# Optimization experiments

Measured on AMD Instinct MI355X. Metric: run time of the kernel, lower is better.

Reference implementation:

```python
import math
import jax, jax.numpy as jnp
import numpy as np

NUM_HEADS = 8


def setup_inputs() -> dict:
    key0 = jax.random.key(0)
    ks = jax.random.split(key0, 11)
    R, C, B, E, Q = 64, 1024, 2, 256, 256
    s = 0.05  # keep pre-softmax scores well-conditioned
    return {
        "query": jax.random.normal(ks[0], (B, Q), jnp.float32),
        "key": jax.random.normal(ks[1], (R, C, B, E), jnp.float32),
        "value": jax.random.normal(ks[2], (R, C, B, E), jnp.float32),
        "Wq": jax.random.normal(ks[3], (E, Q), jnp.float32) * s,
        "bq": jax.random.normal(ks[4], (E,), jnp.float32) * s,
        "Wk": jax.random.normal(ks[5], (E, E), jnp.float32) * s,
        "bk": jax.random.normal(ks[6], (E,), jnp.float32) * s,
        "Wv": jax.random.normal(ks[7], (E, E), jnp.float32) * s,
        "bv": jax.random.normal(ks[8], (E,), jnp.float32) * s,
        "Wo": jax.random.normal(ks[9], (E, E), jnp.float32) * s,
        "bo": jax.random.normal(ks[10], (E,), jnp.float32) * s,
    }


def reference(query, key, value, Wq, bq, Wk, bk, Wv, bv, Wo, bo):
    R, C, B, E = key.shape
    H = NUM_HEADS
    D = E // H
    # main (non-chunked) torch path: align_scaling(query) uses query.size(0) == batch_size
    scaling = (D ** -0.5) / math.sqrt(query.shape[0])
    # projections (torch Linear: x @ W.T + b)
    q = (query @ Wq.T + bq).reshape(B, H, D) * scaling          # [B,H,D]
    k = (key @ Wk.T + bk).reshape(R, C, B, H, D)                # [R,C,B,H,D]
    # tied-row scores: contract over rows r AND head_dim d -> [H,B,C]
    attn_weights = jnp.einsum("nhd,rjnhd->hnj", q, k)
    attn_probs = jax.nn.softmax(attn_weights, axis=-1)          # [H,B,C]
    v = (value @ Wv.T + bv).reshape(R, C, B, H, D)              # [R,C,B,H,D]
    # broadcast probs back per row/column (elementwise scale of v)
    context = jnp.einsum("hnj,rjnhd->rjnhd", attn_probs, v)
    context = context.reshape(R, C, B, E)
    output = context @ Wo.T + bo                                 # [R,C,B,E]
    return output, attn_probs
```

## Files before the change

kernel.cpp:

```cpp
#include <hip/hip_runtime.h>

#define R_DIM 64
#define C_DIM 1024
#define B_DIM 2
#define E_DIM 256
#define Q_DIM 256
#define H_DIM 8
#define D_DIM 32
#define ROW_STRIDE ((size_t)C_DIM * B_DIM * E_DIM)
#define LDS_STRIDE 264
#define OS 260
#define OUT_MAIN ((size_t)R_DIM * C_DIM * B_DIM * E_DIM)

typedef short bf16x8 __attribute__((ext_vector_type(8)));
typedef float f32x4 __attribute__((ext_vector_type(4)));

__device__ __forceinline__ unsigned short f2bf(float x) {
  unsigned int u = __builtin_bit_cast(unsigned int, x);
  u += 0x7FFFu + ((u >> 16) & 1u);
  return (unsigned short)(u >> 16);
}

__global__ void prep_q(const float* __restrict__ query, const float* __restrict__ Wq,
                       const float* __restrict__ bq, float* __restrict__ q_out) {
  int idx = blockIdx.x * 256 + threadIdx.x;
  int n = idx >> 8, e = idx & 255;
  const float4* qr = (const float4*)(query + (size_t)n * Q_DIM);
  const float4* wr = (const float4*)(Wq + (size_t)e * Q_DIM);
  float s = bq[e];
#pragma unroll 8
  for (int k = 0; k < Q_DIM / 4; k++) {
    float4 a = qr[k], b = wr[k];
    s += a.x * b.x + a.y * b.y + a.z * b.z + a.w * b.w;
  }
  q_out[idx] = s * 0.125f;
}

__global__ void prep_w(const float* __restrict__ q, const float* __restrict__ Wk,
                       const float* __restrict__ bk, float* __restrict__ w_out,
                       float* __restrict__ bterm_out) {
  int idx = blockIdx.x * 256 + threadIdx.x;
  int e2 = idx & 255;
  int hn = idx >> 8;
  int n = hn & 1, h = hn >> 1;
  float s = 0.f;
#pragma unroll
  for (int d = 0; d < D_DIM; d++)
    s += q[n * E_DIM + h * D_DIM + d] * Wk[(h * D_DIM + d) * E_DIM + e2];
  w_out[idx] = s;
  if (idx < H_DIM * B_DIM) {
    int nn = idx & 1, hh = idx >> 1;
    float sb = 0.f;
#pragma unroll
    for (int d = 0; d < D_DIM; d++)
      sb += q[nn * E_DIM + hh * D_DIM + d] * bk[hh * D_DIM + d];
    bterm_out[idx] = sb;
  }
}

__global__ void prepack(const float* __restrict__ Wv, const float* __restrict__ Wo,
                        unsigned short* __restrict__ B1p, unsigned short* __restrict__ B2p) {
  int gidx = blockIdx.x * blockDim.x + threadIdx.x;
  const float* src = (gidx < 8192) ? Wv : Wo;
  unsigned short* dst = (gidx < 8192) ? B1p : B2p;
  int li = gidx & 8191;
  int lane = li & 63;
  int pk = li >> 6;
  int ntile = pk >> 3, kstep = pk & 7;
  int row = ntile * 16 + (lane & 15);
  int col0 = kstep * 32 + (lane >> 4) * 8;
  for (int jj = 0; jj < 8; jj++)
    dst[li * 8 + jj] = f2bf(src[row * E_DIM + col0 + jj]);
}

__global__ void scores_kernel(const float* __restrict__ key, const float* __restrict__ w,
                              const float* __restrict__ bterm, float* __restrict__ scores) {
  const int bid = blockIdx.x;
  const int j = bid >> 1, n = bid & 1;
  const int e = threadIdx.x;
  const float* kp = key + ((size_t)j * B_DIM + n) * E_DIM + e;
  float ks = 0.f;
#pragma unroll 8
  for (int r = 0; r < R_DIM; r++) ks += kp[(size_t)r * ROW_STRIDE];

  __shared__ float red[H_DIM][4];
  const int lane = e & 63, wv = e >> 6;
  for (int h = 0; h < H_DIM; h++) {
    float p = ks * w[(h * B_DIM + n) * E_DIM + e];
    for (int off = 32; off > 0; off >>= 1) p += __shfl_down(p, off, 64);
    if (lane == 0) red[h][wv] = p;
  }
  __syncthreads();
  if (e < H_DIM) {
    float s = red[e][0] + red[e][1] + red[e][2] + red[e][3] +
              (float)R_DIM * bterm[e * B_DIM + n];
    scores[(e * B_DIM + n) * C_DIM + j] = s;
  }
}

__global__ void softmax_kernel(const float* __restrict__ scores, float* __restrict__ probs,
                               float* __restrict__ probs_out) {
  const int hn = blockIdx.x;
  const int t = threadIdx.x;
  const float* s = scores + (size_t)hn * C_DIM;
  float v[4];
  float mx = -1e30f;
  for (int i = 0; i < 4; i++) {
    v[i] = s[t + i * 256];
    mx = fmaxf(mx, v[i]);
  }
  __shared__ float sm[4];
  const int lane = t & 63, wv = t >> 6;
  for (int off = 32; off > 0; off >>= 1) mx = fmaxf(mx, __shfl_down(mx, off, 64));
  if (lane == 0) sm[wv] = mx;
  __syncthreads();
  mx = fmaxf(fmaxf(sm[0], sm[1]), fmaxf(sm[2], sm[3]));
  float sum = 0.f;
  for (int i = 0; i < 4; i++) {
    v[i] = expf(v[i] - mx);
    sum += v[i];
  }
  for (int off = 32; off > 0; off >>= 1) sum += __shfl_down(sum, off, 64);
  __syncthreads();
  if (lane == 0) sm[wv] = sum;
  __syncthreads();
  sum = sm[0] + sm[1] + sm[2] + sm[3];
  float inv = 1.0f / sum;
  for (int i = 0; i < 4; i++) {
    float p = v[i] * inv;
    probs[(size_t)hn * C_DIM + t + i * 256] = p;
    probs_out[(size_t)hn * C_DIM + t + i * 256] = p;
  }
}

union SmemT {
  unsigned short tile[64 * LDS_STRIDE];
  float otile[32 * OS];
};

__global__ __launch_bounds__(256, 4) void fused_pv(
    const float* __restrict__ value, const unsigned short* __restrict__ B1p,
    const unsigned short* __restrict__ B2p, const float* __restrict__ bv,
    const float* __restrict__ bo, const float* __restrict__ probs,
    float* __restrict__ out) {
  __shared__ SmemT sm;
  const int bid = blockIdx.x;
  const int j = bid >> 1, n = bid & 1;
  const int t = threadIdx.x;
  const int lane = t & 63;
  const int wv = t >> 6;
  const int l15 = lane & 15;
  const int quad = lane >> 4;

  const float* vbase = value + ((size_t)j * B_DIM + n) * E_DIM;
#pragma unroll
  for (int row = wv; row < 64; row += 4) {
    const float4 v4 = *(((const float4*)(vbase + (size_t)row * ROW_STRIDE)) + lane);
    ushort4 u;
    u.x = f2bf(v4.x); u.y = f2bf(v4.y); u.z = f2bf(v4.z); u.w = f2bf(v4.w);
    *(ushort4*)(&sm.tile[row * LDS_STRIDE + lane * 4]) = u;
  }
  __syncthreads();

  f32x4 acc[4][4];
  const f32x4 zero = {0.f, 0.f, 0.f, 0.f};
#pragma unroll
  for (int mt = 0; mt < 4; mt++)
#pragma unroll
    for (int nt = 0; nt < 4; nt++) acc[mt][nt] = zero;

#pragma unroll
  for (int ks = 0; ks < 8; ks++) {
    bf16x8 a[4], b[4];
#pragma unroll
    for (int mt = 0; mt < 4; mt++)
      a[mt] = *(const bf16x8*)(&sm.tile[(mt * 16 + l15) * LDS_STRIDE + ks * 32 + quad * 8]);
#pragma unroll
    for (int nt = 0; nt < 4; nt++)
      b[nt] = ((const bf16x8*)B1p)[((wv * 4 + nt) * 8 + ks) * 64 + lane];
#pragma unroll
    for (int mt = 0; mt < 4; mt++)
#pragma unroll
      for (int nt = 0; nt < 4; nt++)
        acc[mt][nt] = __builtin_amdgcn_mfma_f32_16x16x32_bf16(a[mt], b[nt], acc[mt][nt], 0, 0, 0);
  }

  const float p0 = probs[((size_t)(2 * wv) * B_DIM + n) * C_DIM + j];
  const float p1 = probs[((size_t)(2 * wv + 1) * B_DIM + n) * C_DIM + j];

  __syncthreads();
#pragma unroll
  for (int nt = 0; nt < 4; nt++) {
    const int e = wv * 64 + nt * 16 + l15;
    const float bias = bv[e];
    const float p = (nt < 2) ? p0 : p1;
#pragma unroll
    for (int mt = 0; mt < 4; mt++) {
#pragma unroll
      for (int i = 0; i < 4; i++) {
        int row = mt * 16 + quad * 4 + i;
        sm.tile[row * LDS_STRIDE + e] = f2bf((acc[mt][nt][i] + bias) * p);
      }
      acc[mt][nt] = zero;
    }
  }
  __syncthreads();

#pragma unroll
  for (int ks = 0; ks < 8; ks++) {
    bf16x8 a[4], b[4];
#pragma unroll
    for (int mt = 0; mt < 4; mt++)
      a[mt] = *(const bf16x8*)(&sm.tile[(mt * 16 + l15) * LDS_STRIDE + ks * 32 + quad * 8]);
#pragma unroll
    for (int nt = 0; nt < 4; nt++)
      b[nt] = ((const bf16x8*)B2p)[((wv * 4 + nt) * 8 + ks) * 64 + lane];
#pragma unroll
    for (int mt = 0; mt < 4; mt++)
#pragma unroll
      for (int nt = 0; nt < 4; nt++)
        acc[mt][nt] = __builtin_amdgcn_mfma_f32_16x16x32_bf16(a[mt], b[nt], acc[mt][nt], 0, 0, 0);
  }

  float* obase = out + ((size_t)j * B_DIM + n) * E_DIM;
#pragma unroll
  for (int h2 = 0; h2 < 2; h2++) {
    __syncthreads();
#pragma unroll
    for (int mt = 2 * h2; mt < 2 * h2 + 2; mt++) {
#pragma unroll
      for (int nt = 0; nt < 4; nt++) {
        const int e = wv * 64 + nt * 16 + l15;
        const float bias = bo[e];
#pragma unroll
        for (int i = 0; i < 4; i++) {
          int lr = (mt - 2 * h2) * 16 + quad * 4 + i;
          sm.otile[lr * OS + e] = acc[mt][nt][i] + bias;
        }
      }
    }
    __syncthreads();
#pragma unroll
    for (int it = 0; it < 8; it++) {
      int idx = it * 256 + t;
      int lr = idx >> 6;
      int f4 = idx & 63;
      float4 v = *(const float4*)(&sm.otile[lr * OS + f4 * 4]);
      *(float4*)(&obase[(size_t)(h2 * 32 + lr) * ROW_STRIDE + f4 * 4]) = v;
    }
  }
}

extern "C" void kernel_launch(void* const* d_in, const int* in_sizes, int n_in,
                              void* d_out, int out_size, void* d_ws, size_t ws_size,
                              hipStream_t stream) {
  const float* query = (const float*)d_in[0];
  const float* key   = (const float*)d_in[1];
  const float* value = (const float*)d_in[2];
  const float* Wq = (const float*)d_in[3];
  const float* bq = (const float*)d_in[4];
  const float* Wk = (const float*)d_in[5];
  const float* bk = (const float*)d_in[6];
  const float* Wv = (const float*)d_in[7];
  const float* bv = (const float*)d_in[8];
  const float* Wo = (const float*)d_in[9];
  const float* bo = (const float*)d_in[10];
  float* out = (float*)d_out;

  float* ws_f = (float*)d_ws;
  float* w_ = ws_f;
  float* bterm_ = ws_f + 4096;
  float* scores_ = ws_f + 4112;
  float* q_ = scores_;
  float* probs_ = ws_f + 20496;
  unsigned short* B1p = (unsigned short*)((char*)d_ws + 147520);
  unsigned short* B2p = (unsigned short*)((char*)d_ws + 147520 + 131072);

  prep_q<<<dim3(2), dim3(256), 0, stream>>>(query, Wq, bq, q_);
  prep_w<<<dim3(16), dim3(256), 0, stream>>>(q_, Wk, bk, w_, bterm_);
  prepack<<<dim3(64), dim3(256), 0, stream>>>(Wv, Wo, B1p, B2p);
  scores_kernel<<<dim3(C_DIM * B_DIM), dim3(256), 0, stream>>>(key, w_, bterm_, scores_);
  softmax_kernel<<<dim3(H_DIM * B_DIM), dim3(256), 0, stream>>>(scores_, probs_,
                                                                out + OUT_MAIN);
  fused_pv<<<dim3(C_DIM * B_DIM), dim3(256), 0, stream>>>(value, B1p, B2p, bv, bo,
                                                          probs_, out);
}
```

Baseline: 405.4 us.

## Widen fused_pv to 512 threads, swizzle LDS, vectorize key reduction, merge prep kernels

Runs the fused projection kernel with 8 waves per block, each owning one head's 32 output columns, which halves per-wave accumulators and lets each wave use a single probability. Replaces padded LDS rows with XOR/rotation-style column swizzles to avoid bank conflicts while saving LDS. The scores kernel now sums key rows with float4 loads split across waves and reduces through shared memory. The weight prep and prepack kernels are merged into one launch. Risks include more synchronisation per block and swizzle index overhead.

```diff
diff --git a/kernel.cpp b/kernel.cpp
--- a/kernel.cpp
+++ b/kernel.cpp
@@ -8,8 +8,6 @@
 #define H_DIM 8
 #define D_DIM 32
 #define ROW_STRIDE ((size_t)C_DIM * B_DIM * E_DIM)
-#define LDS_STRIDE 264
-#define OS 260
 #define OUT_MAIN ((size_t)R_DIM * C_DIM * B_DIM * E_DIM)
 
 typedef short bf16x8 __attribute__((ext_vector_type(8)));
@@ -36,65 +34,74 @@
   q_out[idx] = s * 0.125f;
 }
 
-__global__ void prep_w(const float* __restrict__ q, const float* __restrict__ Wk,
-                       const float* __restrict__ bk, float* __restrict__ w_out,
-                       float* __restrict__ bterm_out) {
-  int idx = blockIdx.x * 256 + threadIdx.x;
-  int e2 = idx & 255;
-  int hn = idx >> 8;
-  int n = hn & 1, h = hn >> 1;
-  float s = 0.f;
-#pragma unroll
-  for (int d = 0; d < D_DIM; d++)
-    s += q[n * E_DIM + h * D_DIM + d] * Wk[(h * D_DIM + d) * E_DIM + e2];
-  w_out[idx] = s;
-  if (idx < H_DIM * B_DIM) {
-    int nn = idx & 1, hh = idx >> 1;
-    float sb = 0.f;
+__global__ void prep_w_pack(const float* __restrict__ q, const float* __restrict__ Wk,
+                            const float* __restrict__ bk, float* __restrict__ w_out,
+                            float* __restrict__ bterm_out,
+                            const float* __restrict__ Wv, const float* __restrict__ Wo,
+                            unsigned short* __restrict__ B1p, unsigned short* __restrict__ B2p) {
+  if (blockIdx.x < 16) {
+    int idx = blockIdx.x * 256 + threadIdx.x;
+    int e2 = idx & 255;
+    int hn = idx >> 8;
+    int n = hn & 1, h = hn >> 1;
+    float s = 0.f;
 #pragma unroll
     for (int d = 0; d < D_DIM; d++)
-      sb += q[nn * E_DIM + hh * D_DIM + d] * bk[hh * D_DIM + d];
-    bterm_out[idx] = sb;
-  }
-}
-
-__global__ void prepack(const float* __restrict__ Wv, const float* __restrict__ Wo,
-                        unsigned short* __restrict__ B1p, unsigned short* __restrict__ B2p) {
-  int gidx = blockIdx.x * blockDim.x + threadIdx.x;
-  const float* src = (gidx < 8192) ? Wv : Wo;
-  unsigned short* dst = (gidx < 8192) ? B1p : B2p;
-  int li = gidx & 8191;
-  int lane = li & 63;
-  int pk = li >> 6;
-  int ntile = pk >> 3, kstep = pk & 7;
-  int row = ntile * 16 + (lane & 15);
-  int col0 = kstep * 32 + (lane >> 4) * 8;
-  for (int jj = 0; jj < 8; jj++)
-    dst[li * 8 + jj] = f2bf(src[row * E_DIM + col0 + jj]);
+      s += q[n * E_DIM + h * D_DIM + d] * Wk[(h * D_DIM + d) * E_DIM + e2];
+    w_out[idx] = s;
+    if (idx < H_DIM * B_DIM) {
+      int nn = idx & 1, hh = idx >> 1;
+      float sb = 0.f;
+#pragma unroll
+      for (int d = 0; d < D_DIM; d++)
+        sb += q[nn * E_DIM + hh * D_DIM + d] * bk[hh * D_DIM + d];
+      bterm_out[idx] = sb;
+    }
+  } else {
+    int gidx = (blockIdx.x - 16) * 256 + threadIdx.x;
+    const float* src = (gidx < 8192) ? Wv : Wo;
+    unsigned short* dst = (gidx < 8192) ? B1p : B2p;
+    int li = gidx & 8191;
+    int lane = li & 63;
+    int pk = li >> 6;
+    int ntile = pk >> 3, kstep = pk & 7;
+    int row = ntile * 16 + (lane & 15);
+    int col0 = kstep * 32 + (lane >> 4) * 8;
+    for (int jj = 0; jj < 8; jj++)
+      dst[li * 8 + jj] = f2bf(src[row * E_DIM + col0 + jj]);
+  }
 }
 
 __global__ void scores_kernel(const float* __restrict__ key, const float* __restrict__ w,
                               const float* __restrict__ bterm, float* __restrict__ scores) {
   const int bid = blockIdx.x;
   const int j = bid >> 1, n = bid & 1;
-  const int e = threadIdx.x;
-  const float* kp = key + ((size_t)j * B_DIM + n) * E_DIM + e;
-  float ks = 0.f;
-#pragma unroll 8
-  for (int r = 0; r < R_DIM; r++) ks += kp[(size_t)r * ROW_STRIDE];
+  const int t = threadIdx.x;
+  const int lane = t & 63, wv = t >> 6;
+
+  const float4* kp = (const float4*)(key + ((size_t)j * B_DIM + n) * E_DIM) + lane;
+  float4 ks4 = {0.f, 0.f, 0.f, 0.f};
+#pragma unroll
+  for (int r = wv; r < R_DIM; r += 4) {
+    float4 v = kp[(size_t)r * (ROW_STRIDE / 4)];
+    ks4.x += v.x; ks4.y += v.y; ks4.z += v.z; ks4.w += v.w;
+  }
+  __shared__ float red4[4][E_DIM];
+  *(float4*)(&red4[wv][lane * 4]) = ks4;
+  __syncthreads();
+  float ks = red4[0][t] + red4[1][t] + red4[2][t] + red4[3][t];
 
   __shared__ float red[H_DIM][4];
-  const int lane = e & 63, wv = e >> 6;
   for (int h = 0; h < H_DIM; h++) {
-    float p = ks * w[(h * B_DIM + n) * E_DIM + e];
+    float p = ks * w[(h * B_DIM + n) * E_DIM + t];
     for (int off = 32; off > 0; off >>= 1) p += __shfl_down(p, off, 64);
     if (lane == 0) red[h][wv] = p;
   }
   __syncthreads();
-  if (e < H_DIM) {
-    float s = red[e][0] + red[e][1] + red[e][2] + red[e][3] +
-              (float)R_DIM * bterm[e * B_DIM + n];
-    scores[(e * B_DIM + n) * C_DIM + j] = s;
+  if (t < H_DIM) {
+    float s = red[t][0] + red[t][1] + red[t][2] + red[t][3] +
+              (float)R_DIM * bterm[t * B_DIM + n];
+    scores[(t * B_DIM + n) * C_DIM + j] = s;
   }
 }
 
@@ -133,12 +140,12 @@
   }
 }
 
-union SmemT {
-  unsigned short tile[64 * LDS_STRIDE];
-  float otile[32 * OS];
+union __align__(16) SmemT {
+  unsigned short tile[64 * 256];
+  float otile[32 * 256];
 };
 
-__global__ __launch_bounds__(256, 4) void fused_pv(
+__global__ __launch_bounds__(512, 6) void fused_pv(
     const float* __restrict__ value, const unsigned short* __restrict__ B1p,
     const unsigned short* __restrict__ B2p, const float* __restrict__ bv,
     const float* __restrict__ bo, const float* __restrict__ probs,
@@ -154,52 +161,56 @@
 
   const float* vbase = value + ((size_t)j * B_DIM + n) * E_DIM;
 #pragma unroll
-  for (int row = wv; row < 64; row += 4) {
+  for (int row = wv; row < 64; row += 8) {
     const float4 v4 = *(((const float4*)(vbase + (size_t)row * ROW_STRIDE)) + lane);
     ushort4 u;
     u.x = f2bf(v4.x); u.y = f2bf(v4.y); u.z = f2bf(v4.z); u.w = f2bf(v4.w);
-    *(ushort4*)(&sm.tile[row * LDS_STRIDE + lane * 4]) = u;
-  }
-  __syncthreads();
-
-  f32x4 acc[4][4];
+    const int col = (lane * 4 + ((row & 12) << 2)) & 255;
+    *(ushort4*)(&sm.tile[row * 256 + col]) = u;
+  }
+  __syncthreads();
+
+  f32x4 acc[4][2];
   const f32x4 zero = {0.f, 0.f, 0.f, 0.f};
 #pragma unroll
   for (int mt = 0; mt < 4; mt++)
 #pragma unroll
-    for (int nt = 0; nt < 4; nt++) acc[mt][nt] = zero;
+    for (int nt = 0; nt < 2; nt++) acc[mt][nt] = zero;
+
+  const int arot = (l15 & 12) << 2;
 
 #pragma unroll
   for (int ks = 0; ks < 8; ks++) {
-    bf16x8 a[4], b[4];
+    bf16x8 a[4], b[2];
 #pragma unroll
     for (int mt = 0; mt < 4; mt++)
-      a[mt] = *(const bf16x8*)(&sm.tile[(mt * 16 + l15) * LDS_STRIDE + ks * 32 + quad * 8]);
-#pragma unroll
-    for (int nt = 0; nt < 4; nt++)
-      b[nt] = ((const bf16x8*)B1p)[((wv * 4 + nt) * 8 + ks) * 64 + lane];
+      a[mt] = *(const bf16x8*)(&sm.tile[(mt * 16 + l15) * 256 +
+                                        ((ks * 32 + quad * 8 + arot) & 255)]);
+#pragma unroll
+    for (int nt = 0; nt < 2; nt++)
+      b[nt] = ((const bf16x8*)B1p)[((wv * 2 + nt) * 8 + ks) * 64 + lane];
 #pragma unroll
     for (int mt = 0; mt < 4; mt++)
 #pragma unroll
-      for (int nt = 0; nt < 4; nt++)
+      for (int nt = 0; nt < 2; nt++)
         acc[mt][nt] = __builtin_amdgcn_mfma_f32_16x16x32_bf16(a[mt], b[nt], acc[mt][nt], 0, 0, 0);
   }
 
-  const float p0 = probs[((size_t)(2 * wv) * B_DIM + n) * C_DIM + j];
-  const float p1 = probs[((size_t)(2 * wv + 1) * B_DIM + n) * C_DIM + j];
-
-  __syncthreads();
-#pragma unroll
-  for (int nt = 0; nt < 4; nt++) {
-    const int e = wv * 64 + nt * 16 + l15;
+  const float p = probs[((size_t)wv * B_DIM + n) * C_DIM + j];
+
+  __syncthreads();
+  const int erot = quad << 4;
+#pragma unroll
+  for (int nt = 0; nt < 2; nt++) {
+    const int e = wv * 32 + nt * 16 + l15;
     const float bias = bv[e];
-    const float p = (nt < 2) ? p0 : p1;
+    const int ecol = (e + erot) & 255;
 #pragma unroll
     for (int mt = 0; mt < 4; mt++) {
 #pragma unroll
       for (int i = 0; i < 4; i++) {
         int row = mt * 16 + quad * 4 + i;
-        sm.tile[row * LDS_STRIDE + e] = f2bf((acc[mt][nt][i] + bias) * p);
+        sm.tile[row * 256 + ecol] = f2bf((acc[mt][nt][i] + bias) * p);
       }
       acc[mt][nt] = zero;
     }
@@ -208,44 +219,48 @@
 
 #pragma unroll
   for (int ks = 0; ks < 8; ks++) {
-    bf16x8 a[4], b[4];
+    bf16x8 a[4], b[2];
 #pragma unroll
     for (int mt = 0; mt < 4; mt++)
-      a[mt] = *(const bf16x8*)(&sm.tile[(mt * 16 + l15) * LDS_STRIDE + ks * 32 + quad * 8]);
-#pragma unroll
-    for (int nt = 0; nt < 4; nt++)
-      b[nt] = ((const bf16x8*)B2p)[((wv * 4 + nt) * 8 + ks) * 64 + lane];
+      a[mt] = *(const bf16x8*)(&sm.tile[(mt * 16 + l15) * 256 +
+                                        ((ks * 32 + quad * 8 + arot) & 255)]);
+#pragma unroll
+    for (int nt = 0; nt < 2; nt++)
+      b[nt] = ((const bf16x8*)B2p)[((wv * 2 + nt) * 8 + ks) * 64 + lane];
 #pragma unroll
     for (int mt = 0; mt < 4; mt++)
 #pragma unroll
-      for (int nt = 0; nt < 4; nt++)
+      for (int nt = 0; nt < 2; nt++)
         acc[mt][nt] = __builtin_amdgcn_mfma_f32_16x16x32_bf16(a[mt], b[nt], acc[mt][nt], 0, 0, 0);
   }
 
   float* obase = out + ((size_t)j * B_DIM + n) * E_DIM;
+  const int orot = quad << 3;
 #pragma unroll
   for (int h2 = 0; h2 < 2; h2++) {
     __syncthreads();
 #pragma unroll
     for (int mt = 2 * h2; mt < 2 * h2 + 2; mt++) {
 #pragma unroll
-      for (int nt = 0; nt < 4; nt++) {
-        const int e = wv * 64 + nt * 16 + l15;
+      for (int nt = 0; nt < 2; nt++) {
+        const int e = wv * 32 + nt * 16 + l15;
         const float bias = bo[e];
+        const int ecol = (e + orot) & 255;
 #pragma unroll
         for (int i = 0; i < 4; i++) {
           int lr = (mt - 2 * h2) * 16 + quad * 4 + i;
-          sm.otile[lr * OS + e] = acc[mt][nt][i] + bias;
+          sm.otile[lr * 256 + ecol] = acc[mt][nt][i] + bias;
         }
       }
     }
     __syncthreads();
 #pragma unroll
-    for (int it = 0; it < 8; it++) {
-      int idx = it * 256 + t;
+    for (int it = 0; it < 4; it++) {
+      int idx = it * 512 + t;
       int lr = idx >> 6;
       int f4 = idx & 63;
-      float4 v = *(const float4*)(&sm.otile[lr * OS + f4 * 4]);
+      int col = (f4 * 4 + ((lr & 12) << 1)) & 255;
+      float4 v = *(const float4*)(&sm.otile[lr * 256 + col]);
       *(float4*)(&obase[(size_t)(h2 * 32 + lr) * ROW_STRIDE + f4 * 4]) = v;
     }
   }
@@ -277,11 +292,10 @@
   unsigned short* B2p = (unsigned short*)((char*)d_ws + 147520 + 131072);
 
   prep_q<<<dim3(2), dim3(256), 0, stream>>>(query, Wq, bq, q_);
-  prep_w<<<dim3(16), dim3(256), 0, stream>>>(q_, Wk, bk, w_, bterm_);
-  prepack<<<dim3(64), dim3(256), 0, stream>>>(Wv, Wo, B1p, B2p);
+  prep_w_pack<<<dim3(80), dim3(256), 0, stream>>>(q_, Wk, bk, w_, bterm_, Wv, Wo, B1p, B2p);
   scores_kernel<<<dim3(C_DIM * B_DIM), dim3(256), 0, stream>>>(key, w_, bterm_, scores_);
   softmax_kernel<<<dim3(H_DIM * B_DIM), dim3(256), 0, stream>>>(scores_, probs_,
                                                                 out + OUT_MAIN);
-  fused_pv<<<dim3(C_DIM * B_DIM), dim3(256), 0, stream>>>(value, B1p, B2p, bv, bo,
+  fused_pv<<<dim3(C_DIM * B_DIM), dim3(512), 0, stream>>>(value, B1p, B2p, bv, bo,
                                                           probs_, out);
 }
```

Measured after the change: 391.5 us. 1.04x faster.
